# Optimization experiments

Measured on AMD Instinct MI355X. Metric: run time of the kernel, lower is better.

## Reference

```python
import jax, jax.numpy as jnp
import numpy as np

DIM = 1024
SEQ_LEN = 4096
K = 256
HEADS = 16
DIM_HEAD = DIM // HEADS  # 64
BATCH = 4


def setup_inputs() -> dict:
    key = jax.random.key(0)
    ks = jax.random.split(key, 8)
    x = jax.random.normal(ks[0], (BATCH, SEQ_LEN, DIM), dtype=jnp.float32)
    # nn.Linear weights are [out, in]; y = x @ W.T
    std_lin = 1.0 / np.sqrt(DIM)
    Wq = jax.random.uniform(ks[1], (HEADS * DIM_HEAD, DIM), minval=-std_lin, maxval=std_lin, dtype=jnp.float32)
    Wk = jax.random.uniform(ks[2], (HEADS * DIM_HEAD, DIM), minval=-std_lin, maxval=std_lin, dtype=jnp.float32)
    Wv = jax.random.uniform(ks[3], (HEADS * DIM_HEAD, DIM), minval=-std_lin, maxval=std_lin, dtype=jnp.float32)
    # proj_k/proj_v init_: uniform(-1/sqrt(k), 1/sqrt(k)) on [seq_len, k]
    std_p = 1.0 / np.sqrt(K)
    proj_k = jax.random.uniform(ks[4], (SEQ_LEN, K), minval=-std_p, maxval=std_p, dtype=jnp.float32)
    proj_v = jax.random.uniform(ks[5], (SEQ_LEN, K), minval=-std_p, maxval=std_p, dtype=jnp.float32)
    std_o = 1.0 / np.sqrt(HEADS * DIM_HEAD)
    Wo = jax.random.uniform(ks[6], (DIM, HEADS * DIM_HEAD), minval=-std_o, maxval=std_o, dtype=jnp.float32)
    bo = jax.random.uniform(ks[7], (DIM,), minval=-std_o, maxval=std_o, dtype=jnp.float32)
    return {"x": x, "Wq": Wq, "Wk": Wk, "Wv": Wv, "proj_k": proj_k, "proj_v": proj_v, "Wo": Wo, "bo": bo}


def reference(x, Wq, Wk, Wv, proj_k, proj_v, Wo, bo):
    b, n, d = x.shape
    h, dh, k = HEADS, DIM_HEAD, K
    # q/k/v projections
    q = jnp.einsum('bnd,ed->bne', x, Wq)            # [b, n, h*dh]
    keys = jnp.einsum('bnd,ed->bne', x, Wk)         # [b, n, h*dh]
    vals = jnp.einsum('bnd,ed->bne', x, Wv)         # [b, n, h*dh]
    # low-rank projection along sequence: [b, n, e] x [n, k] -> [b, k, e]
    keys = jnp.einsum('bne,nk->bke', keys, proj_k[:n])
    vals = jnp.einsum('bne,nk->bke', vals, proj_v[:n])
    # split heads
    q = q.reshape(b, n, h, dh).transpose(0, 2, 1, 3)        # [b, h, n, dh]
    keys = keys.reshape(b, k, h, dh).transpose(0, 2, 1, 3)  # [b, h, k, dh]
    vals = vals.reshape(b, k, h, dh).transpose(0, 2, 1, 3)  # [b, h, k, dh]
    dots = jnp.einsum('bhnd,bhkd->bhnk', q, keys) * (dh ** -0.5)
    attn = jax.nn.softmax(dots, axis=-1)
    out = jnp.einsum('bhnk,bhkd->bhnd', attn, vals)
    out = out.transpose(0, 2, 1, 3).reshape(b, n, h * dh)
    return jnp.einsum('bne,oe->bno', out, Wo) + bo
```

## Files before the change

### kernel.cpp

```cpp
#include <hip/hip_runtime.h>
#include <hip/hip_bf16.h>
#include <stdint.h>

typedef unsigned short u16;
typedef __attribute__((ext_vector_type(8))) short bf16x8;
typedef __attribute__((ext_vector_type(4))) float f32x4;

#define DEV __device__ __forceinline__

DEV u16 f2bf(float f) {
  union { float f; unsigned u; } v; v.f = f;
  unsigned r = (v.u + 0x7fffu + ((v.u >> 16) & 1u)) >> 16;
  return (u16)r;
}

DEV unsigned pk2(float lo, float hi) {
  union { __hip_bfloat162 h; unsigned u; } c;
  c.h = __float22bfloat162_rn(make_float2(lo, hi));
  return c.u;
}

DEV f32x4 mfma16(bf16x8 a, bf16x8 b, f32x4 c) {
  return __builtin_amdgcn_mfma_f32_16x16x32_bf16(a, b, c, 0, 0, 0);
}

DEV void gload_lds16(const u16* g, u16* l) {
  __builtin_amdgcn_global_load_lds((const __attribute__((address_space(1))) void*)g,
                                   (__attribute__((address_space(3))) void*)l, 16, 0, 0);
}

#define QSCALE 0.18033688011112042f

__global__ void cvt_xpose_kernel(const float* __restrict__ src, u16* __restrict__ dst_rm,
                                 u16* __restrict__ dst_tp, int R, int C,
                                 long zS, long zRM, long zTP) {
  __shared__ u16 tile[64][72];
  src += (size_t)blockIdx.z * zS;
  dst_tp += (size_t)blockIdx.z * zTP;
  int r0 = blockIdx.y * 64, c0 = blockIdx.x * 64;
  int tr = threadIdx.x >> 2, tc = (threadIdx.x & 3) * 16;
  const float* s = src + (size_t)(r0 + tr) * C + c0 + tc;
  u16 loc[16];
#pragma unroll
  for (int q = 0; q < 4; ++q) {
    float4 v = ((const float4*)s)[q];
    loc[q * 4 + 0] = f2bf(v.x); loc[q * 4 + 1] = f2bf(v.y);
    loc[q * 4 + 2] = f2bf(v.z); loc[q * 4 + 3] = f2bf(v.w);
  }
#pragma unroll
  for (int i = 0; i < 16; ++i) tile[tr][tc + i] = loc[i];
  if (dst_rm) {
    u16* d = dst_rm + (size_t)blockIdx.z * zRM + (size_t)(r0 + tr) * C + c0 + tc;
    *(bf16x8*)d = *(const bf16x8*)&loc[0];
    *(bf16x8*)(d + 8) = *(const bf16x8*)&loc[8];
  }
  __syncthreads();
  u16 tmp[16];
#pragma unroll
  for (int i = 0; i < 16; ++i) tmp[i] = tile[tc + i][tr];
  u16* d = dst_tp + (size_t)(c0 + tr) * R + r0 + tc;
  *(bf16x8*)d = *(const bf16x8*)&tmp[0];
  *(bf16x8*)(d + 8) = *(const bf16x8*)&tmp[8];
}

__global__ void cvt_w4_kernel(const float* __restrict__ s0, const float* __restrict__ s1,
                              const float* __restrict__ s2, const float* __restrict__ s3,
                              u16* __restrict__ d0, u16* __restrict__ d1,
                              u16* __restrict__ d2, u16* __restrict__ d3) {
  const float* s; u16* d;
  switch (blockIdx.y) {
    case 0: s = s0; d = d0; break;
    case 1: s = s1; d = d1; break;
    case 2: s = s2; d = d2; break;
    default: s = s3; d = d3; break;
  }
  int i = blockIdx.x * 256 + threadIdx.x;
  float4 v = ((const float4*)s)[i];
  ushort4 o; o.x = f2bf(v.x); o.y = f2bf(v.y); o.z = f2bf(v.z); o.w = f2bf(v.w);
  ((ushort4*)d)[i] = o;
}

__global__ void reduce4_kernel(const float* __restrict__ part, u16* __restrict__ out) {
  int i = blockIdx.x * 256 + threadIdx.x;
  const float4* p = (const float4*)part;
  float4 a = p[i], b = p[i + 524288], c = p[i + 1048576], d = p[i + 1572864];
  ushort4 o;
  o.x = f2bf(a.x + b.x + c.x + d.x);
  o.y = f2bf(a.y + b.y + c.y + d.y);
  o.z = f2bf(a.z + b.z + c.z + d.z);
  o.w = f2bf(a.w + b.w + c.w + d.w);
  ((ushort4*)out)[i] = o;
}

template<int OMODE>
__global__ __launch_bounds__(256, 4)
void gemm_bt_kernel(const u16* __restrict__ A, const u16* __restrict__ Bt,
                    const u16* __restrict__ Bt2, void* __restrict__ Cout,
                    u16* __restrict__ CoutT, const float* __restrict__ bias, float cscale,
                    int ldA, int ldB, int ldC, int Klen,
                    long zA, long zB, long zC, int bMod, long kChunk) {
  __shared__ __align__(16) u16 smA[2][128 * 32];
  __shared__ __align__(16) u16 smB[2][128 * 32];
  const int t = threadIdx.x;
  const int lane = t & 63, wave = t >> 6;
  const int wm = wave & 1, wn = wave >> 1;
  const int g = lane >> 4, r = lane & 15;
  const int id = (blockIdx.y << 3) | blockIdx.x;
  const int s = (id & 7) * gridDim.y + (id >> 3);
  const int bx = s & 7, by = s >> 3;
  const int z = blockIdx.z;
  const int b = z % bMod, kc = z / bMod;
  const u16* Ab = A + (size_t)b * zA + (size_t)kc * kChunk;
  const u16* Bbase = (Bt2 && (b & 1)) ? Bt2 : Bt;
  const u16* Bb = Bbase + (size_t)b * zB + (size_t)kc * kChunk;
  const int m0 = by * 128, n0 = bx * 128;
  const int srow = t >> 2;
  const int lslot = ((t & 3) + 4 - ((srow >> 1) & 3)) & 3;

  f32x4 acc[4][4];
#pragma unroll
  for (int m = 0; m < 4; ++m)
#pragma unroll
    for (int n = 0; n < 4; ++n) acc[m][n] = f32x4{0.f, 0.f, 0.f, 0.f};

  auto STAGE = [&](int buf, int k0) {
#pragma unroll
    for (int p = 0; p < 2; ++p) {
      int row = p * 64 + srow;
      gload_lds16(Ab + (size_t)(m0 + row) * ldA + k0 + lslot * 8, &smA[buf][p * 2048 + wave * 512]);
      gload_lds16(Bb + (size_t)(n0 + row) * ldB + k0 + lslot * 8, &smB[buf][p * 2048 + wave * 512]);
    }
  };

  const int nt = Klen >> 5;
  STAGE(0, 0);
  __syncthreads();
  int cur = 0;
  for (int it = 0; it < nt; ++it) {
    if (it + 1 < nt) STAGE(cur ^ 1, (it + 1) << 5);
    bf16x8 af[4], bfr[4];
#pragma unroll
    for (int m = 0; m < 4; ++m) {
      int row = wm * 64 + m * 16 + r;
      int ps = (g + (row >> 1)) & 3;
      af[m] = *(const bf16x8*)&smA[cur][row * 32 + ps * 8];
    }
#pragma unroll
    for (int n = 0; n < 4; ++n) {
      int row = wn * 64 + n * 16 + r;
      int ps = (g + (row >> 1)) & 3;
      bfr[n] = *(const bf16x8*)&smB[cur][row * 32 + ps * 8];
    }
#pragma unroll
    for (int m = 0; m < 4; ++m)
#pragma unroll
      for (int n = 0; n < 4; ++n)
        acc[m][n] = mfma16(af[m], bfr[n], acc[m][n]);
    __syncthreads();
    cur ^= 1;
  }

  if constexpr (OMODE == 0) {
    u16* C = (u16*)Cout + (size_t)z * zC;
#pragma unroll
    for (int n = 0; n < 4; ++n) {
      int col = n0 + wn * 64 + n * 16 + r;
#pragma unroll
      for (int m = 0; m < 4; ++m) {
        int rowb = m0 + wm * 64 + m * 16 + 4 * g;
#pragma unroll
        for (int rr = 0; rr < 4; ++rr)
          C[(size_t)(rowb + rr) * ldC + col] = f2bf(acc[m][n][rr] * cscale);
      }
    }
  } else if constexpr (OMODE == 3) {
    if ((z & 1) == 0) {
      u16* C = (u16*)Cout + (size_t)(z >> 1) * zC;
#pragma unroll
      for (int n = 0; n < 4; ++n) {
        int col = n0 + wn * 64 + n * 16 + r;
#pragma unroll
        for (int m = 0; m < 4; ++m) {
          int rowb = m0 + wm * 64 + m * 16 + 4 * g;
#pragma unroll
          for (int rr = 0; rr < 4; ++rr)
            C[(size_t)(rowb + rr) * ldC + col] = f2bf(acc[m][n][rr]);
        }
      }
    } else {
      u16* C = CoutT + (size_t)(z >> 1) * zC;
#pragma unroll
      for (int n = 0; n < 4; ++n) {
        int col = n0 + wn * 64 + n * 16 + r;
#pragma unroll
        for (int m = 0; m < 4; ++m) {
          int rowb = m0 + wm * 64 + m * 16 + 4 * g;
          ushort4 o;
          o.x = f2bf(acc[m][n][0]); o.y = f2bf(acc[m][n][1]);
          o.z = f2bf(acc[m][n][2]); o.w = f2bf(acc[m][n][3]);
          *(ushort4*)&C[(size_t)col * 256 + rowb] = o;
        }
      }
    }
  } else {
    float* C = (float*)Cout + (size_t)z * zC;
#pragma unroll
    for (int n = 0; n < 4; ++n) {
      int col = n0 + wn * 64 + n * 16 + r;
      float bv = (OMODE == 1) ? bias[col] : 0.f;
#pragma unroll
      for (int m = 0; m < 4; ++m) {
        int rowb = m0 + wm * 64 + m * 16 + 4 * g;
#pragma unroll
        for (int rr = 0; rr < 4; ++rr)
          C[(size_t)(rowb + rr) * ldC + col] = acc[m][n][rr] + bv;
      }
    }
  }
}

#define PHASE(bA, bB, MH, NH, STAGE_STMT, WAITMODE)                                     \
  do {                                                                                  \
    bf16x8 af[4][2], bfv[2][2];                                                         \
    _Pragma("unroll")                                                                   \
    for (int mi = 0; mi < 4; ++mi) {                                                    \
      const u16* rp = (bA) + ((MH) * 128 + aoff + mi * 16) * 64;                        \
      af[mi][0] = *(const bf16x8*)&rp[(g ^ rm) * 8];                                    \
      af[mi][1] = *(const bf16x8*)&rp[((4 + g) ^ rm) * 8];                              \
    }                                                                                   \
    _Pragma("unroll")                                                                   \
    for (int ni = 0; ni < 2; ++ni) {                                                    \
      const u16* rp = (bB) + ((NH) * 128 + boff + ni * 16) * 64;                        \
      bfv[ni][0] = *(const bf16x8*)&rp[(g ^ rm) * 8];                                   \
      bfv[ni][1] = *(const bf16x8*)&rp[((4 + g) ^ rm) * 8];                             \
    }                                                                                   \
    STAGE_STMT;                                                                         \
    __builtin_amdgcn_s_barrier();                                                       \
    __builtin_amdgcn_sched_barrier(0);                                                  \
    __builtin_amdgcn_s_setprio(1);                                                      \
    _Pragma("unroll")                                                                   \
    for (int mi = 0; mi < 4; ++mi)                                                      \
      _Pragma("unroll")                                                                 \
      for (int ni = 0; ni < 2; ++ni) {                                                  \
        acc[(MH)*4+mi][(NH)*2+ni] = mfma16(af[mi][0], bfv[ni][0], acc[(MH)*4+mi][(NH)*2+ni]); \
        acc[(MH)*4+mi][(NH)*2+ni] = mfma16(af[mi][1], bfv[ni][1], acc[(MH)*4+mi][(NH)*2+ni]); \
      }                                                                                 \
    __builtin_amdgcn_s_setprio(0);                                                      \
    if ((WAITMODE) == 1) asm volatile("s_waitcnt vmcnt(4)" ::: "memory");               \
    if ((WAITMODE) == 2) asm volatile("s_waitcnt vmcnt(0)" ::: "memory");               \
    __builtin_amdgcn_s_barrier();                                                       \
    __builtin_amdgcn_sched_barrier(0);                                                  \
  } while (0)

template<int OMODE>
__global__ __launch_bounds__(512, 1)
void gemm256_kernel(const u16* __restrict__ A, const u16* __restrict__ Bt,
                    void* __restrict__ Cout, const float* __restrict__ bias,
                    float cscale, int ldA, int ldB, int ldC, int Klen) {
  __shared__ __align__(16) u16 lds[65536];
  const int t = threadIdx.x;
  const int lane = t & 63, wave = t >> 6;
  const int g = lane >> 4, r = lane & 15, rm = r & 7;
  const int wm = wave >> 2, wn = wave & 3;
  const int id = blockIdx.y * 4 + blockIdx.x;
  const int sw = (id & 7) * 32 + (id >> 3);
  const int bx = sw & 3, by = sw >> 2;
  const int m0 = by * 256, n0 = bx * 256;

  const int trow = t >> 3, tslot = t & 7;
  const int sslot = tslot ^ (trow & 7);
  const u16* Asrc = A + (size_t)(m0 + trow) * ldA + sslot * 8;
  const u16* Bsrc = Bt + sslot * 8;
  const int bRow0 = n0 + (trow >> 5) * 64 + (trow & 31);
  const int bRow1 = n0 + (2 + (trow >> 5)) * 64 + (trow & 31);

  u16* const A0 = lds;
  u16* const A1 = lds + 16384;
  u16* const B0 = lds + 32768;
  u16* const B1 = lds + 49152;

  auto stageA = [&](u16* buf, int h, int k0) {
    u16* d = buf + h * 8192 + t * 8;
    const u16* s0 = Asrc + (size_t)(h * 64) * ldA + k0;
    gload_lds16(s0, d);
    gload_lds16(s0 + (size_t)128 * ldA, d + 4096);
  };
  auto stageB = [&](u16* buf, int h, int k0) {
    u16* d = buf + h * 8192 + t * 8;
    gload_lds16(Bsrc + (size_t)(bRow0 + h * 32) * ldB + k0, d);
    gload_lds16(Bsrc + (size_t)(bRow1 + h * 32) * ldB + k0, d + 4096);
  };

  const int aoff = wm * 64 + r;
  const int boff = wn * 32 + r;

  f32x4 acc[8][4];
#pragma unroll
  for (int m = 0; m < 8; ++m)
#pragma unroll
    for (int n = 0; n < 4; ++n) acc[m][n] = f32x4{0.f, 0.f, 0.f, 0.f};

  stageA(A0, 0, 0); stageB(B0, 0, 0); stageA(A0, 1, 0); stageB(B0, 1, 0);
  stageA(A1, 0, 64); stageB(B1, 0, 64);
  asm volatile("s_waitcnt vmcnt(4)" ::: "memory");
  __builtin_amdgcn_s_barrier();
  __builtin_amdgcn_sched_barrier(0);

  const int nt = Klen >> 6;
  for (int j = 0; j < (nt >> 1); ++j) {
    const int ta = 2 * j, tb = ta + 1;
    const int more = (ta + 2 < nt);
    const int kb = tb * 64, kn = (ta + 2) * 64, kn2 = (tb + 2) * 64;
    PHASE(A0, B0, 0, 0, stageA(A1, 1, kb), 0);
    PHASE(A0, B0, 0, 1, stageB(B1, 1, kb), 0);
    PHASE(A0, B0, 1, 0, if (more) stageA(A0, 0, kn), 0);
    PHASE(A0, B0, 1, 1, if (more) stageB(B0, 0, kn), more ? 1 : 2);
    PHASE(A1, B1, 0, 0, if (more) stageA(A0, 1, kn), 0);
    PHASE(A1, B1, 0, 1, if (more) stageB(B0, 1, kn), 0);
    PHASE(A1, B1, 1, 0, if (more) stageA(A1, 0, kn2), 0);
    PHASE(A1, B1, 1, 1, if (more) stageB(B1, 0, kn2), more ? 1 : 2);
  }

  if constexpr (OMODE == 0) {
    u16* C = (u16*)Cout;
#pragma unroll
    for (int n = 0; n < 4; ++n) {
      int col = n0 + wn * 64 + n * 16 + r;
#pragma unroll
      for (int m = 0; m < 8; ++m) {
        int rowb = m0 + wm * 128 + m * 16 + 4 * g;
#pragma unroll
        for (int rr = 0; rr < 4; ++rr)
          C[(size_t)(rowb + rr) * ldC + col] = f2bf(acc[m][n][rr] * cscale);
      }
    }
  } else {
    float* C = (float*)Cout;
#pragma unroll
    for (int n = 0; n < 4; ++n) {
      int col = n0 + wn * 64 + n * 16 + r;
      float bv = bias[col];
#pragma unroll
      for (int m = 0; m < 8; ++m) {
        int rowb = m0 + wm * 128 + m * 16 + 4 * g;
#pragma unroll
        for (int rr = 0; rr < 4; ++rr)
          C[(size_t)(rowb + rr) * ldC + col] = acc[m][n][rr] + bv;
      }
    }
  }
}

__global__ __launch_bounds__(256, 4)
void attn_kernel(const u16* __restrict__ Q, const u16* __restrict__ Kl,
                 const u16* __restrict__ VT, u16* __restrict__ Out) {
  __shared__ __align__(16) u16 sm[20480];
  const int t = threadIdx.x, lane = t & 63, w = t >> 6;
  const int g = lane >> 4, r = lane & 15;
  const int id = (blockIdx.y << 6) | blockIdx.x;
  const int s = (id & 7) * (gridDim.y << 3) + (id >> 3);
  const int b = blockIdx.z, h = s >> 6, n0 = (s & 63) * 64;
  const u16* Kb = Kl + (size_t)b * 262144 + h * 64;
  const u16* Vb = VT + (size_t)b * 262144 + (size_t)(h * 64) * 256;
  u16* vbase = sm + 16384;

  const int vd = t >> 2;
  const int vsl = (t & 3) ^ (vd & 3);
  auto stage_slice = [&](int kk, int buf) {
    gload_lds16(Vb + (size_t)vd * 256 + kk * 32 + vsl * 8, vbase + buf * 2048 + w * 512);
  };

#pragma unroll
  for (int p = 0; p < 8; ++p) {
    int row = p * 32 + (t >> 3);
    int ls = ((t & 7) + 8 - (row & 7)) & 7;
    gload_lds16(Kb + (size_t)row * 1024 + ls * 8, sm + p * 2048 + w * 512);
  }
  stage_slice(0, 0);
  stage_slice(1, 1);
  const int qrow = n0 + w * 16 + r;
  const u16* Qp = Q + ((size_t)(b * 4096 + qrow)) * 1024 + h * 64 + g * 8;
  bf16x8 aq0 = *(const bf16x8*)Qp;
  bf16x8 aq1 = *(const bf16x8*)(Qp + 32);
  __syncthreads();

  f32x4 dotv[16];
#pragma unroll
  for (int kf = 0; kf < 16; ++kf) {
    int row = kf * 16 + r;
    bf16x8 kb0 = *(const bf16x8*)&sm[row * 64 + ((g + row) & 7) * 8];
    bf16x8 kb1 = *(const bf16x8*)&sm[row * 64 + ((4 + g + row) & 7) * 8];
    f32x4 d = f32x4{0.f, 0.f, 0.f, 0.f};
    d = mfma16(kb0, aq0, d);
    d = mfma16(kb1, aq1, d);
    dotv[kf] = d;
  }
  __syncthreads();

  float mx = -3.4e38f;
#pragma unroll
  for (int kf = 0; kf < 16; ++kf)
    mx = fmaxf(mx, fmaxf(fmaxf(dotv[kf][0], dotv[kf][1]), fmaxf(dotv[kf][2], dotv[kf][3])));
  mx = fmaxf(mx, __shfl_xor(mx, 16, 64));
  mx = fmaxf(mx, __shfl_xor(mx, 32, 64));
  float ssum = 0.f;
#pragma unroll
  for (int kf = 0; kf < 16; ++kf)
#pragma unroll
    for (int j = 0; j < 4; ++j) {
      float p = exp2f(dotv[kf][j] - mx);
      dotv[kf][j] = p;
      ssum += p;
    }
  ssum += __shfl_xor(ssum, 16, 64);
  ssum += __shfl_xor(ssum, 32, 64);
  const float inv = 1.f / ssum;

  const int q16 = w * 16 + r;
  const int qx = (q16 & 7) << 3;
#pragma unroll
  for (int kf = 0; kf < 16; ++kf) {
    uint2 val;
    val.x = pk2(dotv[kf][0] * inv, dotv[kf][1] * inv);
    val.y = pk2(dotv[kf][2] * inv, dotv[kf][3] * inv);
    *(uint2*)&sm[(q16 * 256 + kf * 16 + 4 * g) ^ qx] = val;
  }

  f32x4 oacc[4];
#pragma unroll
  for (int df = 0; df < 4; ++df) oacc[df] = f32x4{0.f, 0.f, 0.f, 0.f};
#pragma unroll
  for (int kk = 0; kk < 8; ++kk) {
    bf16x8 ap = *(const bf16x8*)&sm[(q16 * 256 + kk * 32 + g * 8) ^ qx];
    const u16* vb = vbase + (kk & 1) * 2048;
#pragma unroll
    for (int df = 0; df < 4; ++df) {
      int d = df * 16 + r;
      bf16x8 bv = *(const bf16x8*)&vb[d * 32 + (g ^ (d & 3)) * 8];
      oacc[df] = mfma16(ap, bv, oacc[df]);
    }
    if (kk < 7) {
      __syncthreads();
      if (kk < 6) stage_slice(kk + 2, kk & 1);
    }
  }
#pragma unroll
  for (int df = 0; df < 4; ++df)
#pragma unroll
    for (int rr = 0; rr < 4; ++rr) {
      int orow = n0 + w * 16 + 4 * g + rr;
      int ocol = h * 64 + df * 16 + r;
      Out[((size_t)(b * 4096 + orow)) * 1024 + ocol] = f2bf(oacc[df][rr]);
    }
}

extern "C" void kernel_launch(void* const* d_in, const int* in_sizes, int n_in,
                              void* d_out, int out_size, void* d_ws, size_t ws_size,
                              hipStream_t stream) {
  const float* x  = (const float*)d_in[0];
  const float* Wq = (const float*)d_in[1];
  const float* Wk = (const float*)d_in[2];
  const float* Wv = (const float*)d_in[3];
  const float* pk = (const float*)d_in[4];
  const float* pv = (const float*)d_in[5];
  const float* Wo = (const float*)d_in[6];
  const float* bo = (const float*)d_in[7];

  u16* ws = (u16*)d_ws;
  u16* xbf   = ws;
  u16* xT    = xbf + 16777216;
  u16* wqb   = xT + 16777216;
  u16* wkb   = wqb + 1048576;
  u16* wvb   = wkb + 1048576;
  u16* wob   = wvb + 1048576;
  u16* projT = wob + 1048576;
  u16* Qb    = projT + 2097152;
  u16* xp    = Qb + 16777216;
  u16* klow  = xp + 2097152;
  u16* vT    = klow + 1048576;
  u16* aout  = xbf;
  float* xp_part = (float*)Qb;

  cvt_xpose_kernel<<<dim3(16, 64, 4), 256, 0, stream>>>(x, xbf, xT, 4096, 1024,
                                                        4194304, 4194304, 4194304);
  cvt_w4_kernel<<<dim3(1024, 4), 256, 0, stream>>>(Wq, Wk, Wv, Wo, wqb, wkb, wvb, wob);
  cvt_xpose_kernel<<<dim3(4, 64, 1), 256, 0, stream>>>(pk, nullptr, projT, 4096, 256, 0, 0, 0);
  cvt_xpose_kernel<<<dim3(4, 64, 1), 256, 0, stream>>>(pv, nullptr, projT + 1048576, 4096, 256, 0, 0, 0);
  gemm_bt_kernel<2><<<dim3(8, 4, 16), 256, 0, stream>>>(
      projT, xT, nullptr, (void*)xp_part, nullptr, nullptr, 1.f,
      4096, 4096, 1024, 1024, 0, 4194304, 524288, 4, 1024);
  reduce4_kernel<<<2048, 256, 0, stream>>>(xp_part, xp);
  gemm_bt_kernel<3><<<dim3(8, 2, 8), 256, 0, stream>>>(
      xp, wkb, wvb, (void*)klow, vT, nullptr, 1.f,
      1024, 1024, 1024, 1024, 262144, 0, 262144, 8, 0);
  gemm256_kernel<0><<<dim3(4, 64), 512, 0, stream>>>(
      xbf, wqb, (void*)Qb, nullptr, QSCALE, 1024, 1024, 1024, 1024);
  attn_kernel<<<dim3(64, 16, 4), 256, 0, stream>>>(Qb, klow, vT, aout);
  gemm256_kernel<1><<<dim3(4, 64), 512, 0, stream>>>(
      aout, wob, d_out, bo, 1.f, 1024, 1024, 1024, 1024);
}
```

Before: 226.1 us.

## Reuse LDS fragments across MFMA phases and stage GEMM epilogue through LDS

The 256x256 GEMM main loop now keeps A and B register fragments across phases, so each fragment is read from LDS once per tile instead of being re-read in every phase. The epilogue for both bf16 and fp32 outputs writes accumulators into a per-wave swizzled LDS tile and then stores to global memory with 16-byte row-contiguous vector writes, replacing scattered 2- or 4-byte stores. The aim is to cut LDS read traffic and make output writes coalesced. The cost is higher register pressure from the extra fragment arrays and an extra LDS round trip in the epilogue.

```diff
diff --git a/kernel.cpp b/kernel.cpp
--- a/kernel.cpp
+++ b/kernel.cpp
@@ -219,22 +219,8 @@
   }
 }
 
-#define PHASE(bA, bB, MH, NH, STAGE_STMT, WAITMODE)                                     \
+#define MFMA_CLUSTER(MH, NH, AF, BV)                                                    \
   do {                                                                                  \
-    bf16x8 af[4][2], bfv[2][2];                                                         \
-    _Pragma("unroll")                                                                   \
-    for (int mi = 0; mi < 4; ++mi) {                                                    \
-      const u16* rp = (bA) + ((MH) * 128 + aoff + mi * 16) * 64;                        \
-      af[mi][0] = *(const bf16x8*)&rp[(g ^ rm) * 8];                                    \
-      af[mi][1] = *(const bf16x8*)&rp[((4 + g) ^ rm) * 8];                              \
-    }                                                                                   \
-    _Pragma("unroll")                                                                   \
-    for (int ni = 0; ni < 2; ++ni) {                                                    \
-      const u16* rp = (bB) + ((NH) * 128 + boff + ni * 16) * 64;                        \
-      bfv[ni][0] = *(const bf16x8*)&rp[(g ^ rm) * 8];                                   \
-      bfv[ni][1] = *(const bf16x8*)&rp[((4 + g) ^ rm) * 8];                             \
-    }                                                                                   \
-    STAGE_STMT;                                                                         \
     __builtin_amdgcn_s_barrier();                                                       \
     __builtin_amdgcn_sched_barrier(0);                                                  \
     __builtin_amdgcn_s_setprio(1);                                                      \
@@ -242,12 +228,16 @@
     for (int mi = 0; mi < 4; ++mi)                                                      \
       _Pragma("unroll")                                                                 \
       for (int ni = 0; ni < 2; ++ni) {                                                  \
-        acc[(MH)*4+mi][(NH)*2+ni] = mfma16(af[mi][0], bfv[ni][0], acc[(MH)*4+mi][(NH)*2+ni]); \
-        acc[(MH)*4+mi][(NH)*2+ni] = mfma16(af[mi][1], bfv[ni][1], acc[(MH)*4+mi][(NH)*2+ni]); \
+        acc[(MH)*4+mi][(NH)*2+ni] = mfma16(AF[mi][0], BV[ni][0], acc[(MH)*4+mi][(NH)*2+ni]); \
+        acc[(MH)*4+mi][(NH)*2+ni] = mfma16(AF[mi][1], BV[ni][1], acc[(MH)*4+mi][(NH)*2+ni]); \
       }                                                                                 \
     __builtin_amdgcn_s_setprio(0);                                                      \
-    if ((WAITMODE) == 1) asm volatile("s_waitcnt vmcnt(4)" ::: "memory");               \
-    if ((WAITMODE) == 2) asm volatile("s_waitcnt vmcnt(0)" ::: "memory");               \
+  } while (0)
+
+#define ENDBAR(W)                                                                       \
+  do {                                                                                  \
+    if ((W) == 1) asm volatile("s_waitcnt vmcnt(4)" ::: "memory");                      \
+    if ((W) == 2) asm volatile("s_waitcnt vmcnt(0)" ::: "memory");                      \
     __builtin_amdgcn_s_barrier();                                                       \
     __builtin_amdgcn_sched_barrier(0);                                                  \
   } while (0)
@@ -294,6 +284,23 @@
   const int aoff = wm * 64 + r;
   const int boff = wn * 32 + r;
 
+  auto loadA = [&](bf16x8 af[4][2], const u16* base, int MH) {
+#pragma unroll
+    for (int mi = 0; mi < 4; ++mi) {
+      const u16* rp = base + (MH * 128 + aoff + mi * 16) * 64;
+      af[mi][0] = *(const bf16x8*)&rp[(g ^ rm) * 8];
+      af[mi][1] = *(const bf16x8*)&rp[((4 + g) ^ rm) * 8];
+    }
+  };
+  auto loadB = [&](bf16x8 bv[2][2], const u16* base, int NH) {
+#pragma unroll
+    for (int ni = 0; ni < 2; ++ni) {
+      const u16* rp = base + (NH * 128 + boff + ni * 16) * 64;
+      bv[ni][0] = *(const bf16x8*)&rp[(g ^ rm) * 8];
+      bv[ni][1] = *(const bf16x8*)&rp[((4 + g) ^ rm) * 8];
+    }
+  };
+
   f32x4 acc[8][4];
 #pragma unroll
   for (int m = 0; m < 8; ++m)
@@ -311,41 +318,76 @@
     const int ta = 2 * j, tb = ta + 1;
     const int more = (ta + 2 < nt);
     const int kb = tb * 64, kn = (ta + 2) * 64, kn2 = (tb + 2) * 64;
-    PHASE(A0, B0, 0, 0, stageA(A1, 1, kb), 0);
-    PHASE(A0, B0, 0, 1, stageB(B1, 1, kb), 0);
-    PHASE(A0, B0, 1, 0, if (more) stageA(A0, 0, kn), 0);
-    PHASE(A0, B0, 1, 1, if (more) stageB(B0, 0, kn), more ? 1 : 2);
-    PHASE(A1, B1, 0, 0, if (more) stageA(A0, 1, kn), 0);
-    PHASE(A1, B1, 0, 1, if (more) stageB(B0, 1, kn), 0);
-    PHASE(A1, B1, 1, 0, if (more) stageA(A1, 0, kn2), 0);
-    PHASE(A1, B1, 1, 1, if (more) stageB(B1, 0, kn2), more ? 1 : 2);
+    bf16x8 af[4][2], bv0[2][2], bv1[2][2];
+    loadA(af, A0, 0); loadB(bv0, B0, 0);
+    stageA(A1, 1, kb);
+    MFMA_CLUSTER(0, 0, af, bv0); ENDBAR(0);
+    loadB(bv1, B0, 1);
+    stageB(B1, 1, kb);
+    MFMA_CLUSTER(0, 1, af, bv1); ENDBAR(0);
+    loadA(af, A0, 1);
+    if (more) stageA(A0, 0, kn);
+    MFMA_CLUSTER(1, 0, af, bv0); ENDBAR(0);
+    if (more) stageB(B0, 0, kn);
+    MFMA_CLUSTER(1, 1, af, bv1); ENDBAR(more ? 1 : 2);
+    loadA(af, A1, 0); loadB(bv0, B1, 0);
+    if (more) stageA(A0, 1, kn);
+    MFMA_CLUSTER(0, 0, af, bv0); ENDBAR(0);
+    loadB(bv1, B1, 1);
+    if (more) stageB(B0, 1, kn);
+    MFMA_CLUSTER(0, 1, af, bv1); ENDBAR(0);
+    loadA(af, A1, 1);
+    if (more) stageA(A1, 0, kn2);
+    MFMA_CLUSTER(1, 0, af, bv0); ENDBAR(0);
+    if (more) stageB(B1, 0, kn2);
+    MFMA_CLUSTER(1, 1, af, bv1); ENDBAR(more ? 1 : 2);
   }
 
   if constexpr (OMODE == 0) {
-    u16* C = (u16*)Cout;
-#pragma unroll
-    for (int n = 0; n < 4; ++n) {
-      int col = n0 + wn * 64 + n * 16 + r;
-#pragma unroll
-      for (int m = 0; m < 8; ++m) {
-        int rowb = m0 + wm * 128 + m * 16 + 4 * g;
-#pragma unroll
-        for (int rr = 0; rr < 4; ++rr)
-          C[(size_t)(rowb + rr) * ldC + col] = f2bf(acc[m][n][rr] * cscale);
-      }
+    u16* myT = lds + wave * 8192;
+#pragma unroll
+    for (int m = 0; m < 8; ++m)
+#pragma unroll
+      for (int n = 0; n < 4; ++n)
+#pragma unroll
+        for (int rr = 0; rr < 4; ++rr) {
+          int rl = m * 16 + 4 * g + rr;
+          int cl = n * 16 + r;
+          myT[rl * 64 + (((cl >> 3) ^ (rl & 7)) << 3) + (cl & 7)] = f2bf(acc[m][n][rr] * cscale);
+        }
+    u16* Cg = (u16*)Cout + (size_t)(m0 + wm * 128) * ldC + n0 + wn * 64;
+#pragma unroll
+    for (int i = 0; i < 16; ++i) {
+      int idx = i * 64 + lane;
+      int row = idx >> 3, c8 = idx & 7;
+      bf16x8 v = *(const bf16x8*)&myT[row * 64 + ((c8 ^ (row & 7)) << 3)];
+      *(bf16x8*)&Cg[(size_t)row * ldC + c8 * 8] = v;
     }
   } else {
-    float* C = (float*)Cout;
-#pragma unroll
-    for (int n = 0; n < 4; ++n) {
-      int col = n0 + wn * 64 + n * 16 + r;
-      float bv = bias[col];
-#pragma unroll
-      for (int m = 0; m < 8; ++m) {
-        int rowb = m0 + wm * 128 + m * 16 + 4 * g;
-#pragma unroll
-        for (int rr = 0; rr < 4; ++rr)
-          C[(size_t)(rowb + rr) * ldC + col] = acc[m][n][rr] + bv;
+    float* myF = (float*)lds + wave * 4096;
+    float bvn[4];
+#pragma unroll
+    for (int n = 0; n < 4; ++n) bvn[n] = bias[n0 + wn * 64 + n * 16 + r];
+    float* Cg = (float*)Cout + (size_t)(m0 + wm * 128) * ldC + n0 + wn * 64;
+#pragma unroll
+    for (int half = 0; half < 2; ++half) {
+#pragma unroll
+      for (int m2 = 0; m2 < 4; ++m2)
+#pragma unroll
+        for (int n = 0; n < 4; ++n)
+#pragma unroll
+          for (int rr = 0; rr < 4; ++rr) {
+            int rl = m2 * 16 + 4 * g + rr;
+            int cl = n * 16 + r;
+            myF[rl * 64 + (((cl >> 2) ^ (rl & 15)) << 2) + (cl & 3)] =
+                acc[half * 4 + m2][n][rr] + bvn[n];
+          }
+#pragma unroll
+      for (int i = 0; i < 16; ++i) {
+        int idx = i * 64 + lane;
+        int row = idx >> 4, c4 = idx & 15;
+        float4 v = *(const float4*)&myF[row * 64 + ((c4 ^ (row & 15)) << 2)];
+        *(float4*)&Cg[(size_t)(half * 64 + row) * ldC + c4 * 4] = v;
       }
     }
   }
```

Result: faster. 221.4 us (-2.1%).
